# Optimization experiments

Hardware: AMD Instinct MI355X
Metric: run time of the kernel (lower is better)

Reference implementation:

```python
import jax, jax.numpy as jnp
import numpy as np

BEAM_WIDTH = 16   # beam_width init kwarg
TOP_PATHS = 1     # top_paths init kwarg
NEG = -1.0e30     # log-domain 'zero' (avoid -inf for stable grads)


def _beam_search_single(log_probs):
    """CTC prefix beam search for one example.

    log_probs: (T, V) log-softmax scores; blank is class V-1 (TF convention).
    Returns (decoded, scores): decoded (TOP_PATHS, T) int32 padded with -1,
    scores (TOP_PATHS,) final log-probabilities of the top prefixes.
    Prefix merging is done for the blank/repeat (stay) transitions of each
    beam (the dominant merge in CTC); cross-beam duplicate-prefix merging is
    approximated by pruning, as in common production beam-search kernels.
    """
    T, V = log_probs.shape
    C = V - 1                      # number of non-blank characters
    W = BEAM_WIDTH

    prefixes = jnp.full((W, T), -1, dtype=jnp.int32)
    lengths = jnp.zeros((W,), dtype=jnp.int32)
    p_b = jnp.full((W,), NEG, dtype=log_probs.dtype).at[0].set(0.0)   # log P(prefix, ends in blank)
    p_nb = jnp.full((W,), NEG, dtype=log_probs.dtype)                 # log P(prefix, ends in non-blank)

    def step(state, lp):
        prefixes, lengths, p_b, p_nb = state
        lp_blank = lp[C]
        lp_c = lp[:C]                                   # (C,)
        p_tot = jnp.logaddexp(p_b, p_nb)                # (W,)

        # last character of each beam (-1 if empty prefix)
        last = jnp.take_along_axis(prefixes, jnp.maximum(lengths - 1, 0)[:, None], axis=1)[:, 0]
        last = jnp.where(lengths > 0, last, -1)

        # --- stay candidates: same prefix, via blank or repeated last char ---
        new_p_b = p_tot + lp_blank                      # (W,)
        lp_last = jnp.take(lp_c, jnp.maximum(last, 0))
        new_p_nb_stay = jnp.where(last >= 0, p_nb + lp_last, NEG)
        stay_score = jnp.logaddexp(new_p_b, new_p_nb_stay)

        # --- extend candidates: prefix + c, for every non-blank c ---
        same = jnp.arange(C)[None, :] == last[:, None]  # (W, C)
        base = jnp.where(same, p_b[:, None], p_tot[:, None])
        ext_score = base + lp_c[None, :]                # (W, C) -> new p_nb

        all_scores = jnp.concatenate([stay_score, ext_score.reshape(-1)])  # (W + W*C,)
        top_scores, top_idx = jax.lax.top_k(all_scores, W)

        is_stay = top_idx < W
        beam = jnp.where(is_stay, top_idx, (top_idx - W) // C)
        char = jnp.where(is_stay, 0, (top_idx - W) % C).astype(jnp.int32)

        par_pref = prefixes[beam]                       # (W, T)
        par_len = lengths[beam]                         # (W,)
        pos = jnp.arange(T)[None, :]
        ext_pref = jnp.where(pos == par_len[:, None], char[:, None], par_pref)

        new_prefixes = jnp.where(is_stay[:, None], par_pref, ext_pref)
        new_lengths = jnp.where(is_stay, par_len, par_len + 1)
        new_pb = jnp.where(is_stay, new_p_b[beam], NEG)
        new_pnb = jnp.where(is_stay, new_p_nb_stay[beam], top_scores)
        return (new_prefixes, new_lengths, new_pb, new_pnb), None

    (prefixes, lengths, p_b, p_nb), _ = jax.lax.scan(step, (prefixes, lengths, p_b, p_nb), log_probs)

    final_scores = jnp.logaddexp(p_b, p_nb)             # (W,)
    best_scores, best_idx = jax.lax.top_k(final_scores, TOP_PATHS)
    return prefixes[best_idx], best_scores


def setup_inputs() -> dict:
    key = jax.random.key(0)
    # (batch, time, num_classes) logits, blank = last class (TF convention)
    inputs = jax.random.normal(key, (512, 512, 96), dtype=jnp.float32)
    return {"inputs": inputs}


def reference(inputs):
    # tf.nn.ctc_beam_search_decoder normalizes logits internally
    log_probs = jax.nn.log_softmax(inputs, axis=-1)        # (B, T, V)
    decoded, scores = jax.vmap(_beam_search_single)(log_probs)
    # decoded: (B, TOP_PATHS, T) token ids padded with -1 (stands in for the
    # string-table detokenize); probability = exp(log_probability) as in call()
    probability = jnp.exp(scores)                          # (B, TOP_PATHS)
    return decoded, probability
```

## Files before the change

kernel.cpp:

```cpp
#include <hip/hip_runtime.h>
#include <math.h>

#define NBATCH 512
#define TSTEPS 512
#define VCLS   96
#define CCLS   95
#define BWID   16
#define VPAD   104
#define NEGF   (-1e30f)

typedef unsigned long long u64;
typedef unsigned int u32;

__device__ __forceinline__ float exp_xla(float x){
    x = fminf(x, 88.3762626647950f);
    x = fmaxf(x, -88.3762626647949f);
    float t = __fadd_rn(__fmul_rn(x, 1.44269504088896341f), 0.5f);
    float m = floorf(t);
    float r = __fadd_rn(__fmul_rn(m, -0.693359375f), x);
    r = __fadd_rn(__fmul_rn(m, 2.12194440e-4f), r);
    float y = 1.9875691500E-4f;
    y = __fadd_rn(__fmul_rn(y, r), 1.3981999507E-3f);
    y = __fadd_rn(__fmul_rn(y, r), 8.3334519073E-3f);
    y = __fadd_rn(__fmul_rn(y, r), 4.1665795894E-2f);
    y = __fadd_rn(__fmul_rn(y, r), 1.6666665459E-1f);
    y = __fadd_rn(__fmul_rn(y, r), 5.0000001201E-1f);
    float r2 = __fmul_rn(r, r);
    y = __fadd_rn(__fmul_rn(y, r2), r);
    y = __fadd_rn(y, 1.0f);
    int n = (int)m;
    unsigned sb = (unsigned)(n + 127);
    float s = __uint_as_float(sb << 23);
    return __fmul_rn(y, s);
}

__device__ __forceinline__ float log_xla(float x){
    unsigned bits = __float_as_uint(x);
    int e = (int)(bits >> 23) - 126;
    float m = __uint_as_float((bits & 0x007FFFFFu) | 0x3F000000u);
    if (m < 0.707106781186547524f){
        e -= 1;
        m = __fsub_rn(__fadd_rn(m, m), 1.0f);
    } else {
        m = __fsub_rn(m, 1.0f);
    }
    float z = __fmul_rn(m, m);
    float p = 7.0376836292E-2f;
    p = __fadd_rn(__fmul_rn(p, m), -1.1514610310E-1f);
    p = __fadd_rn(__fmul_rn(p, m),  1.1676998740E-1f);
    p = __fadd_rn(__fmul_rn(p, m), -1.2420140846E-1f);
    p = __fadd_rn(__fmul_rn(p, m),  1.4249322787E-1f);
    p = __fadd_rn(__fmul_rn(p, m), -1.6668057665E-1f);
    p = __fadd_rn(__fmul_rn(p, m),  2.0000714765E-1f);
    p = __fadd_rn(__fmul_rn(p, m), -2.4999993993E-1f);
    p = __fadd_rn(__fmul_rn(p, m),  3.3333331174E-1f);
    float y = __fmul_rn(m, __fmul_rn(z, p));
    float fe = (float)e;
    y = __fadd_rn(y, __fmul_rn(-2.12194440e-4f, fe));
    y = __fadd_rn(y, __fmul_rn(-0.5f, z));
    float rr = __fadd_rn(m, y);
    rr = __fadd_rn(rr, __fmul_rn(0.693359375f, fe));
    return rr;
}

__device__ __forceinline__ float log1p_xla(float x){
    float u = __fadd_rn(x, 1.0f);
    if (u == 1.0f) return x;
    float lu = log_xla(u);
    float um1 = __fsub_rn(u, 1.0f);
    return __fmul_rn(lu, __fdiv_rn(x, um1));
}

__device__ __forceinline__ float logaddexp_x(float x, float y){
    float amax = fmaxf(x, y);
    float d = __fsub_rn(x, y);
    float e = exp_xla(-fabsf(d));
    float l1p = log1p_xla(e);
    return __fadd_rn(amax, l1p);
}

__device__ __forceinline__ unsigned ford(float f){
    unsigned u = __float_as_uint(f);
    return (u & 0x80000000u) ? ~u : (u | 0x80000000u);
}
__device__ __forceinline__ float unford(u32 u){
    return __uint_as_float((u & 0x80000000u) ? (u ^ 0x80000000u) : ~u);
}

__device__ __forceinline__ double packkey(float sc, int k){
    u64 kb = ((u64)ford(sc) << 31) | ((u64)((~(u32)k) & 0x7FFu) << 20);
    return __longlong_as_double((long long)kb);
}
__device__ __forceinline__ int decodekey(double wk){
    u32 idxinv = (u32)((u64)__double_as_longlong(wk) >> 20) & 0x7FFu;
    return (int)((~idxinv) & 0x7FFu);
}
__device__ __forceinline__ double packlp(float v, int c){
    u64 kb = ((u64)ford(v) << 31) | ((u64)((~(u32)c) & 0x7Fu) << 24);
    return __longlong_as_double((long long)kb);
}

__device__ __forceinline__ void wave_fence(){
    asm volatile("s_waitcnt lgkmcnt(0)" ::: "memory");
    __builtin_amdgcn_sched_barrier(0);
}

template<int CTRL>
__device__ __forceinline__ double dpp_d(double v){
    long long x = __double_as_longlong(v);
    int lo = __builtin_amdgcn_update_dpp((int)(u32)x, (int)(u32)x, CTRL, 0xF, 0xF, false);
    int hi = __builtin_amdgcn_update_dpp((int)(u32)(x >> 32), (int)(u32)(x >> 32), CTRL, 0xF, 0xF, false);
    return __longlong_as_double((long long)(((u64)(u32)hi << 32) | (u32)lo));
}
template<int CTRL>
__device__ __forceinline__ double dmaxd(double v){
    double o = dpp_d<CTRL>(v);
    return fmax(v, o);
}
template<int CTRL>
__device__ __forceinline__ float dmaxf(float v){
    int o = __builtin_amdgcn_update_dpp(__float_as_int(v), __float_as_int(v), CTRL, 0xF, 0xF, false);
    return fmaxf(v, __int_as_float(o));
}
__device__ __forceinline__ double rowmax_d(double v){
    v = dmaxd<0xB1>(v); v = dmaxd<0x4E>(v); v = dmaxd<0x141>(v); v = dmaxd<0x140>(v);
    return v;
}
__device__ __forceinline__ float rowmax_f(float v){
    v = dmaxf<0xB1>(v); v = dmaxf<0x4E>(v); v = dmaxf<0x141>(v); v = dmaxf<0x140>(v);
    return v;
}
template<int CTRL>
__device__ __forceinline__ void dmax2(double& a1, double& a2){
    double p1 = dpp_d<CTRL>(a1);
    double p2 = dpp_d<CTRL>(a2);
    double n1 = fmax(a1, p1);
    double n2 = fmax(fmin(a1, p1), fmax(a2, p2));
    a1 = n1; a2 = n2;
}

__global__ __launch_bounds__(128)
void ctc_beam(const float* __restrict__ in, float* __restrict__ out)
{
    __shared__ __align__(16) float ring[8][2][VPAD];
    __shared__ __align__(8)  float2 srtS[8][2][17];
    __shared__ __align__(16) float evS[4][VPAD];
    __shared__ float lsS[4];
    __shared__ float2 stateF2[2][BWID];
    __shared__ int2   lastlenS[2][BWID];
    __shared__ unsigned short bp[2][TSTEPS][BWID];
    __shared__ float finalsS[2][BWID];

    const int tid  = threadIdx.x;
    const int wid  = tid >> 6;
    const int lane = tid & 63;
    const int rl   = lane & 15;
    const int eh   = (lane >> 4) & 1;
    const int bm   = rl;
    const int unit = lane >> 4;
    const int pex  = unit & 1;
    const int pdt  = unit >> 1;
    const int bex  = blockIdx.x * 2 + eh;
    const int pbex = blockIdx.x * 2 + pex;
    const float* __restrict__ prow = in + (size_t)pbex * TSTEPS * VCLS;

    float pb_r = NEGF, pnb_r = NEGF;
    int last_r = -1, len_r = 0;

    float xv[6], xw[6];

    auto LOADROW = [&](int r, float* dst){
        const float* p = prow + (size_t)r * VCLS + rl;
        #pragma unroll
        for (int j = 0; j < 6; ++j) dst[j] = p[j * 16];
    };
    auto PRODUCE = [&](int buf, const float* x){
        float lm = fmaxf(fmaxf(fmaxf(x[0], x[1]), fmaxf(x[2], x[3])), fmaxf(x[4], x[5]));
        float m = rowmax_f(lm);
        float sh[6];
        #pragma unroll
        for (int j = 0; j < 6; ++j){
            sh[j] = __fsub_rn(x[j], m);
            evS[unit][j * 16 + rl] = exp_xla(sh[j]);
        }
        wave_fence();
        if (rl == 0){
            float s = 0.0f;
            const float4* e4 = (const float4*)evS[unit];
            #pragma unroll
            for (int g = 0; g < 24; ++g){
                float4 w = e4[g];
                s = __fadd_rn(s, w.x); s = __fadd_rn(s, w.y);
                s = __fadd_rn(s, w.z); s = __fadd_rn(s, w.w);
            }
            lsS[unit] = log_xla(s);
        }
        wave_fence();
        float ls = lsS[unit];
        double kk[6];
        #pragma unroll
        for (int j = 0; j < 6; ++j){
            float lp = __fsub_rn(sh[j], ls);
            ring[buf][pex][j * 16 + rl] = lp;
            int c = j * 16 + rl;
            kk[j] = (c == CCLS) ? 0.0 : packlp(lp, c);
        }
        double t0 = fmax(kk[0], kk[1]), t1 = fmax(kk[2], kk[3]), t2 = fmax(kk[4], kk[5]);
        double pl = fmax(fmax(t0, t1), t2);
        #pragma unroll 1
        for (int i = 0; i < 17; ++i){
            double wk = rowmax_d(pl);
            if (rl == 0){
                u64 bits = (u64)__double_as_longlong(wk);
                int c = (int)((~(u32)(bits >> 24)) & 0x7Fu);
                srtS[buf][pex][i] = make_float2(unford((u32)(bits >> 31)), __int_as_float(c));
            }
            long long wkb = __double_as_longlong(wk);
            #pragma unroll
            for (int j = 0; j < 6; ++j)
                kk[j] = (__double_as_longlong(kk[j]) == wkb) ? 0.0 : kk[j];
            double u0 = fmax(kk[0], kk[1]), u1 = fmax(kk[2], kk[3]), u2 = fmax(kk[4], kk[5]);
            pl = fmax(fmax(u0, u1), u2);
        }
    };

    if (wid == 1){
        LOADROW(pdt, xv);
        PRODUCE(pdt, xv);
        LOADROW(2 + pdt, xv);
        PRODUCE(2 + pdt, xv);
        LOADROW(4 + pdt, xv);
        LOADROW(6 + pdt, xw);
    } else {
        pb_r = (bm == 0) ? 0.0f : NEGF;
        pnb_r = NEGF; last_r = -1; len_r = 0;
        if (lane < 32){
            lastlenS[eh][bm] = make_int2(-1, 0);
        }
    }
    __syncthreads();

    auto STEP = [&](int t){
        const float*  __restrict__ lpc = ring[t & 7][eh];
        const float2* __restrict__ srt = srtS[t & 7][eh];

        float sv[17]; int scv[17];
        #pragma unroll
        for (int j = 0; j < 17; ++j){
            float2 e = srt[j];
            sv[j] = e.x; scv[j] = __float_as_int(e.y);
        }
        float lpb = lpc[CCLS];
        float lpl = lpc[(last_r >= 0) ? last_r : 0];

        float pt  = logaddexp_x(pb_r, pnb_r);
        float npb = pt + lpb;
        float stnb = (last_r >= 0) ? (pnb_r + lpl) : NEGF;
        float stay = logaddexp_x(npb, stnb);
        if (lane < 32){
            stateF2[eh][bm] = make_float2(npb, stnb);
        }

        const int idx0 = BWID + bm * CCLS;
        double ins = (last_r >= 0) ? packkey(__fadd_rn(pb_r, lpl), idx0 + last_r) : 0.0;
        double raw[17];
        #pragma unroll
        for (int j = 0; j < 17; ++j)
            raw[j] = packkey(__fadd_rn(pt, sv[j]), idx0 + scv[j]);
        u32 mq = 0;
        #pragma unroll
        for (int j = 0; j < 17; ++j) mq |= (scv[j] == last_r) ? (1u << j) : 0u;
        int tpos = mq ? __builtin_ctz(mq) : 99;
        double st[18];
        {
            double f0 = (0 < tpos) ? raw[0] : raw[1];
            bool g0 = f0 > ins;
            st[0] = g0 ? f0 : ins;
            bool gprev = g0;
            double fprev = f0;
            #pragma unroll
            for (int j = 1; j < 16; ++j){
                double fj = (j < tpos) ? raw[j] : raw[j + 1];
                bool g = fj > ins;
                st[j] = g ? fj : (gprev ? ins : fprev);
                gprev = g; fprev = fj;
            }
        }
        st[16] = 0.0; st[17] = 0.0;

        #pragma unroll
        for (int ph = 0; ph < 4; ++ph){
            #pragma unroll
            for (int j = (ph & 1); j < 15; j += 2){
                double a = st[j], bk = st[j + 1];
                bool sw = a < bk;
                st[j]     = sw ? bk : a;
                st[j + 1] = sw ? a : bk;
            }
        }

        double stay_k = packkey(stay, bm);
        double l1 = fmax(stay_k, st[0]);
        double l2 = fmax(fmin(stay_k, st[0]), st[1]);
        int mysel = 0;
        float myscore = 0.0f;
        #pragma unroll
        for (int r = 0; r < 8; ++r){
            double a1 = l1, a2 = l2;
            dmax2<0xB1>(a1, a2);
            dmax2<0x4E>(a1, a2);
            dmax2<0x141>(a1, a2);
            dmax2<0x140>(a1, a2);
            if (bm == 2 * r){
                mysel = decodekey(a1);
                myscore = unford((u32)((u64)__double_as_longlong(a1) >> 31));
            }
            if (bm == 2 * r + 1){
                mysel = decodekey(a2);
                myscore = unford((u32)((u64)__double_as_longlong(a2) >> 31));
            }
            if (r < 7){
                long long w1 = __double_as_longlong(a1);
                long long w2 = __double_as_longlong(a2);
                bool m0 = (__double_as_longlong(st[0]) == w1) | (__double_as_longlong(st[0]) == w2);
                bool m1 = (__double_as_longlong(st[1]) == w1) | (__double_as_longlong(st[1]) == w2);
                int cnt = (int)m0 + (int)m1;
                #pragma unroll
                for (int j = 0; j < 16; ++j)
                    st[j] = (cnt == 0) ? st[j] : ((cnt == 1) ? st[j + 1] : st[j + 2]);
                bool sm = (__double_as_longlong(stay_k) == w1) | (__double_as_longlong(stay_k) == w2);
                stay_k = sm ? 0.0 : stay_k;
                l1 = fmax(stay_k, st[0]);
                l2 = fmax(fmin(stay_k, st[0]), st[1]);
            }
        }

        wave_fence();
        int nlast, nlen, parent, code;
        float npbV, npnbV;
        {
            int s = mysel;
            if (s < BWID){
                parent = s; code = 0;
                float2 f2 = stateF2[eh][s];
                int2 i2 = lastlenS[eh][s];
                nlast = i2.x; nlen = i2.y;
                npbV = f2.x; npnbV = f2.y;
            } else {
                u32 e = (u32)(s - BWID);
                parent = (int)((e * 44151u) >> 22);
                int c = (int)(e - (u32)parent * 95u);
                code = c + 1;
                nlast = c;
                int2 i2 = lastlenS[eh][parent];
                nlen = i2.y + 1;
                npbV = NEGF;
                npnbV = myscore;
            }
        }
        __builtin_amdgcn_sched_barrier(0);
        pb_r = npbV; pnb_r = npnbV; last_r = nlast; len_r = nlen;
        if (lane < 32){
            lastlenS[eh][bm] = make_int2(nlast, nlen);
            bp[eh][t][bm] = (unsigned short)((parent << 8) | code);
        }
    };

    for (int k = 0; k < TSTEPS / 4; ++k){
        if (wid == 1){
            if (k + 1 < TSTEPS / 4){
                float cx[6], cy[6];
                #pragma unroll
                for (int j = 0; j < 6; ++j){ cx[j] = xv[j]; cy[j] = xw[j]; }
                if (k + 2 < TSTEPS / 4){
                    LOADROW(4 * k + 8 + pdt, xv);
                    LOADROW(4 * k + 10 + pdt, xw);
                }
                #pragma unroll 1
                for (int s = 0; s < 2; ++s){
                    float cc[6];
                    #pragma unroll
                    for (int j = 0; j < 6; ++j) cc[j] = s ? cy[j] : cx[j];
                    PRODUCE((4 * k + 4 + 2 * s + pdt) & 7, cc);
                }
            }
        } else {
            #pragma unroll 1
            for (int s = 0; s < 4; ++s) STEP(4 * k + s);
        }
        __syncthreads();
    }

    if (wid == 0){
        if (lane < 32) finalsS[eh][bm] = logaddexp_x(pb_r, pnb_r);
        wave_fence();
        int bi_loc = 0;
        if (rl == 0 && lane < 32){
            float bv = finalsS[eh][0];
            for (int i = 1; i < BWID; ++i){
                if (finalsS[eh][i] > bv){ bv = finalsS[eh][i]; bi_loc = i; }
            }
            out[(size_t)NBATCH * TSTEPS + bex] = exp_xla(bv);
        }
        int biA = __builtin_amdgcn_readlane(bi_loc, 0);
        int biB = __builtin_amdgcn_readlane(bi_loc, 16);
        int bi = eh ? biB : biA;
        int L  = lastlenS[eh][bi].y;
        if (lane < 32){
            for (int j = L + rl; j < TSTEPS; j += 16) out[(size_t)bex * TSTEPS + j] = -1.0f;
        }
        if (rl == 0 && lane < 32){
            int beam = bi, pos = L;
            for (int t = TSTEPS - 1; t >= 0; --t){
                unsigned short e = bp[eh][t][beam];
                int code = e & 0xFF;
                if (code){ out[(size_t)bex * TSTEPS + (pos - 1)] = (float)(code - 1); pos--; }
                beam = e >> 8;
            }
        }
    }
}

extern "C" void kernel_launch(void* const* d_in, const int* in_sizes, int n_in,
                              void* d_out, int out_size, void* d_ws, size_t ws_size,
                              hipStream_t stream)
{
    const float* in = (const float*)d_in[0];
    float* out = (float*)d_out;
    hipLaunchKernelGGL(ctc_beam, dim3(NBATCH / 2), dim3(128), 0, stream, in, out);
}
```

Measured before the change: 1.702 ms.

## Replace iterative top-2 extraction rounds with bitonic merge of sorted 16-lists across lanes

```diff
diff --git a/kernel.cpp b/kernel.cpp
--- a/kernel.cpp
+++ b/kernel.cpp
@@ -131,12 +131,26 @@
     return v;
 }
 template<int CTRL>
-__device__ __forceinline__ void dmax2(double& a1, double& a2){
-    double p1 = dpp_d<CTRL>(a1);
-    double p2 = dpp_d<CTRL>(a2);
-    double n1 = fmax(a1, p1);
-    double n2 = fmax(fmin(a1, p1), fmax(a2, p2));
-    a1 = n1; a2 = n2;
+__device__ __forceinline__ void merge16(double* s){
+    double b[16];
+    #pragma unroll
+    for (int j = 0; j < 16; ++j) b[j] = dpp_d<CTRL>(s[j]);
+    double c[16];
+    #pragma unroll
+    for (int j = 0; j < 16; ++j) c[j] = fmax(s[j], b[15 - j]);
+    #pragma unroll
+    for (int d = 8; d; d >>= 1){
+        #pragma unroll
+        for (int i = 0; i < 16; ++i){
+            if ((i & d) == 0){
+                double hi = fmax(c[i], c[i + d]);
+                double lo = fmin(c[i], c[i + d]);
+                c[i] = hi; c[i + d] = lo;
+            }
+        }
+    }
+    #pragma unroll
+    for (int j = 0; j < 16; ++j) s[j] = c[j];
 }
 
 __global__ __launch_bounds__(128)
@@ -271,7 +285,7 @@
         #pragma unroll
         for (int j = 0; j < 17; ++j) mq |= (scv[j] == last_r) ? (1u << j) : 0u;
         int tpos = mq ? __builtin_ctz(mq) : 99;
-        double st[18];
+        double st[16];
         {
             double f0 = (0 < tpos) ? raw[0] : raw[1];
             bool g0 = f0 > ins;
@@ -286,7 +300,6 @@
                 gprev = g; fprev = fj;
             }
         }
-        st[16] = 0.0; st[17] = 0.0;
 
         #pragma unroll
         for (int ph = 0; ph < 4; ++ph){
@@ -300,40 +313,35 @@
         }
 
         double stay_k = packkey(stay, bm);
-        double l1 = fmax(stay_k, st[0]);
-        double l2 = fmax(fmin(stay_k, st[0]), st[1]);
-        int mysel = 0;
-        float myscore = 0.0f;
-        #pragma unroll
-        for (int r = 0; r < 8; ++r){
-            double a1 = l1, a2 = l2;
-            dmax2<0xB1>(a1, a2);
-            dmax2<0x4E>(a1, a2);
-            dmax2<0x141>(a1, a2);
-            dmax2<0x140>(a1, a2);
-            if (bm == 2 * r){
-                mysel = decodekey(a1);
-                myscore = unford((u32)((u64)__double_as_longlong(a1) >> 31));
-            }
-            if (bm == 2 * r + 1){
-                mysel = decodekey(a2);
-                myscore = unford((u32)((u64)__double_as_longlong(a2) >> 31));
-            }
-            if (r < 7){
-                long long w1 = __double_as_longlong(a1);
-                long long w2 = __double_as_longlong(a2);
-                bool m0 = (__double_as_longlong(st[0]) == w1) | (__double_as_longlong(st[0]) == w2);
-                bool m1 = (__double_as_longlong(st[1]) == w1) | (__double_as_longlong(st[1]) == w2);
-                int cnt = (int)m0 + (int)m1;
-                #pragma unroll
-                for (int j = 0; j < 16; ++j)
-                    st[j] = (cnt == 0) ? st[j] : ((cnt == 1) ? st[j + 1] : st[j + 2]);
-                bool sm = (__double_as_longlong(stay_k) == w1) | (__double_as_longlong(stay_k) == w2);
-                stay_k = sm ? 0.0 : stay_k;
-                l1 = fmax(stay_k, st[0]);
-                l2 = fmax(fmin(stay_k, st[0]), st[1]);
-            }
-        }
+        double stb[16];
+        {
+            bool gprev = true;
+            double sprev = 0.0;
+            #pragma unroll
+            for (int j = 0; j < 16; ++j){
+                bool g = st[j] > stay_k;
+                stb[j] = g ? st[j] : (gprev ? stay_k : sprev);
+                gprev = g; sprev = st[j];
+            }
+        }
+
+        merge16<0xB1>(stb);
+        merge16<0x4E>(stb);
+        merge16<0x141>(stb);
+        merge16<0x140>(stb);
+
+        double v01[8];
+        #pragma unroll
+        for (int j = 0; j < 8; ++j) v01[j] = (bm & 1) ? stb[2 * j + 1] : stb[2 * j];
+        double v2[4];
+        #pragma unroll
+        for (int j = 0; j < 4; ++j) v2[j] = (bm & 2) ? v01[2 * j + 1] : v01[2 * j];
+        double v4[2];
+        #pragma unroll
+        for (int j = 0; j < 2; ++j) v4[j] = (bm & 4) ? v2[2 * j + 1] : v2[2 * j];
+        double win = (bm & 8) ? v4[1] : v4[0];
+        int mysel = decodekey(win);
+        float myscore = unford((u32)((u64)__double_as_longlong(win) >> 31));
 
         wave_fence();
         int nlast, nlen, parent, code;
```

New measurement: 2.100 ms. 23.4% more time.
